# Kernel tuning notes

Hardware: AMD Instinct MI355X
Metric: run time of the kernel (lower is better)

The kernel has to match this reference:

```python
import jax, jax.numpy as jnp
import numpy as np

# geometry constants (mirrors geo dict in init_kwargs)
N_DETEC_U = 512
VIEWS = 360
N_VOX_X = 128
N_VOX_Y = 128
EXTENT = 1
CHANNEL = 8
RANGE_X = 5            # self.range_x_num
R = 2 * RANGE_X + 1    # 11 interpolation taps per sample


def conv1d(x, w, b):
    # x: [N, Cin, L], w: [Cout, Cin, K], padding=1 (same)
    y = jax.lax.conv_general_dilated(
        x, w, window_strides=(1,), padding=((1, 1),),
        dimension_numbers=("NCH", "OIH", "NCH"))
    return y + b[None, :, None]


def setup_inputs() -> dict:
    key = jax.random.key(0)
    k1, k2, k3, k4, k5, k6 = jax.random.split(key, 6)
    B = 2
    hidden = R * CHANNEL * 2   # 176
    out_ch = R * CHANNEL       # 88
    inp = jax.random.normal(k1, (B, CHANNEL, VIEWS, N_DETEC_U), dtype=jnp.float32)
    # indices live in [0, views*nDetecU - 2) so low_ind+1 / high_ind+1 stay in range
    max_idx = float(VIEWS * N_DETEC_U - 2)
    indices = jax.random.uniform(k2, (N_VOX_X * N_VOX_Y * VIEWS * EXTENT,),
                                 dtype=jnp.float32) * max_idx
    fc1_w = jax.random.normal(k3, (hidden, CHANNEL, 3), dtype=jnp.float32) * 0.05
    fc1_b = jax.random.normal(k4, (hidden,), dtype=jnp.float32) * 0.05
    fc2_w = jax.random.normal(k5, (out_ch, hidden, 3), dtype=jnp.float32) * 0.05
    fc2_b = jax.random.normal(k6, (out_ch,), dtype=jnp.float32) * 0.05
    return {"input": inp, "indices": indices, "fc1_w": fc1_w, "fc1_b": fc1_b,
            "fc2_w": fc2_w, "fc2_b": fc2_b}


def reference(input, indices, fc1_w, fc1_b, fc2_w, fc2_b):
    B, C, V, D = input.shape  # [B, channel, views, nDetecU]
    # ---- Mlp (Conv1d -> GELU -> Conv1d) applied per (batch, view) slice ----
    x = jnp.transpose(input, (0, 2, 1, 3)).reshape(B * V, C, D)  # [B*V, C, D]
    h = jax.nn.gelu(conv1d(x, fc1_w, fc1_b), approximate=False)
    y = conv1d(h, fc2_w, fc2_b)                                   # [B*V, R*C, D]
    y = jnp.transpose(y.reshape(B, V, R * C, D), (0, 2, 1, 3))    # [B, R*C, V, D]
    # split R taps to last axis: [B, C, V, D, R] -> flatten last three
    out = jnp.transpose(y.reshape(B, C, R, V, D), (0, 1, 3, 4, 2)).reshape(B, C, V * D * R)
    L = V * D * R
    # ---- back-projection interpolation index math ----
    idx_low = jnp.floor(indices)
    w = indices - idx_low                       # torch.frac (indices >= 0)
    fw = jnp.floor(w * RANGE_X)
    low_ind = idx_low * R + RANGE_X + fw
    low_w = w * RANGE_X - fw                    # frac(weight * range_x_num)
    high_ind = low_ind + RANGE_X + 1
    high_ind = jnp.where(high_ind >= L - 1, float(L - 2), high_ind)
    li = low_ind.astype(jnp.int32)
    hi = high_ind.astype(jnp.int32)
    low = out[:, :, li] * (1.0 - low_w) + out[:, :, li + 1] * low_w
    high = out[:, :, hi] * (1.0 - low_w) + out[:, :, hi + 1] * low_w
    res = low * (1.0 - w) + high * w            # [B, C, Nvox*views*extent]
    return res.reshape(B, C, N_VOX_X * N_VOX_Y, V * EXTENT)
```

## Files before the change

### kernel.cpp

```cpp
#include <hip/hip_runtime.h>
#include <hip/hip_fp16.h>
#include <math.h>

#define VIEWS  360
#define NDET   512
#define CH     8
#define RR     11
#define HID    176
#define OC     88
#define LPOS   (VIEWS*NDET*RR)
#define NIDX   (128*128*VIEWS)

#define DCHUNK 128
#define NCHUNK (NDET/DCHUNK)
#define HTROWS (DCHUNK+2)
#define HTHALF 192
#define NMT    6
#define NKSTEP 18

typedef _Float16 f16x8 __attribute__((ext_vector_type(8)));
typedef float    f32x4 __attribute__((ext_vector_type(4)));

__device__ __align__(16) _Float16 g_w2a[NKSTEP*NMT*64*8];

__device__ __forceinline__ int swz(int r) { return (r ^ (r >> 3)) & 7; }

__global__ __launch_bounds__(256) void pack_w2(const float* __restrict__ w2)
{
    int idx = blockIdx.x*256 + threadIdx.x;
    if (idx >= NKSTEP*NMT*64*8) return;
    int j     = idx & 7;
    int lane  = (idx >> 3) & 63;
    int t     = idx >> 9;
    int mt    = t % NMT;
    int kstep = t / NMT;
    int kb    = kstep / 3, tap = kstep % 3;
    int o     = mt*16 + (lane & 15);
    int hh    = kb*32 + (lane >> 4)*8 + j;
    float v   = (o < OC && hh < HID) ? w2[(o*HID + hh)*3 + tap] : 0.f;
    g_w2a[idx] = (_Float16)v;
}

__global__ __launch_bounds__(256, 2) void mlp_kernel(
    const float* __restrict__ input,
    const float* __restrict__ w1,
    const float* __restrict__ b1,
    const float* __restrict__ b2,
    __half* __restrict__ ws)
{
    const int v    = blockIdx.x;
    const int b    = blockIdx.y;
    const int tid  = threadIdx.x;
    const int lane = tid & 63;
    const int wv   = tid >> 6;
    const int l15  = lane & 15;
    const int l4   = lane >> 4;

    __shared__ __align__(16) float    x_s[520][8];
    __shared__ __align__(16) _Float16 w1_s[HID][24];
    __shared__ float                  b1_s[HID];
    __shared__ __align__(16) _Float16 hT[HTROWS * HTHALF];

    {
        int4 zi = make_int4(0,0,0,0);
        for (int i = tid; i < (HTROWS*HTHALF*2)/16; i += 256) ((int4*)hT)[i] = zi;
    }
    for (int j = tid; j < CH*NDET; j += 256) {
        int c = j >> 9, d = j & 511;
        x_s[d + 2][c] = input[((b*CH + c)*VIEWS + v)*NDET + d];
    }
    if (tid < 64) {
        int t = tid >> 3;
        int row = (t < 2) ? t : 512 + t;
        x_s[row][tid & 7] = 0.f;
    }
    for (int i = tid; i < HID*24; i += 256) w1_s[i/24][i%24] = (_Float16)w1[i];
    for (int i = tid; i < HID;    i += 256) b1_s[i] = b1[i];

    float accb[NMT][4];
    #pragma unroll
    for (int mt = 0; mt < NMT; ++mt)
        #pragma unroll
        for (int q = 0; q < 4; ++q) {
            int o = mt*16 + l4*4 + q;
            accb[mt][q] = (o < OC) ? b2[o] : 0.f;
        }

    __syncthreads();

    for (int chunk = 0; chunk < NCHUNK; ++chunk) {
        const int d0 = chunk * DCHUNK;

        #pragma unroll 1
        for (int it = 0; it < 3; ++it) {
            int i = it*256 + tid;
            if (i < 726) {
                int oct = i / 33;
                int rg  = i - oct*33;
                int r0  = rg * 4;
                float xr[6][8];
                #pragma unroll
                for (int k = 0; k < 6; ++k) {
                    const float4* xp = (const float4*)(&x_s[d0 + r0 + k][0]);
                    float4 xa = xp[0], xb = xp[1];
                    xr[k][0]=xa.x; xr[k][1]=xa.y; xr[k][2]=xa.z; xr[k][3]=xa.w;
                    xr[k][4]=xb.x; xr[k][5]=xb.y; xr[k][6]=xb.z; xr[k][7]=xb.w;
                }
                f16x8 hout[4];
                #pragma unroll
                for (int hsub = 0; hsub < 8; ++hsub) {
                    int hh = oct*8 + hsub;
                    const f16x8* wp = (const f16x8*)(&w1_s[hh][0]);
                    f16x8 wA = wp[0], wB = wp[1], wC = wp[2];
                    float wr[24];
                    #pragma unroll
                    for (int t = 0; t < 8; ++t) {
                        wr[t] = (float)wA[t]; wr[8+t] = (float)wB[t]; wr[16+t] = (float)wC[t];
                    }
                    float bias = b1_s[hh];
                    #pragma unroll
                    for (int rr = 0; rr < 4; ++rr) {
                        float a = bias;
                        #pragma unroll
                        for (int c = 0; c < CH; ++c) {
                            a += wr[c*3+0] * xr[rr+0][c]
                               + wr[c*3+1] * xr[rr+1][c]
                               + wr[c*3+2] * xr[rr+2][c];
                        }
                        int d = d0 - 1 + r0 + rr;
                        float g = 0.f;
                        if ((unsigned)d < (unsigned)NDET)
                            g = 0.5f * a * (1.0f + erff(a * 0.70710678118654752f));
                        hout[rr][hsub] = (_Float16)g;
                    }
                }
                #pragma unroll
                for (int rr = 0; rr < 4; ++rr) {
                    int r = r0 + rr;
                    if (r < HTROWS) {
                        int g = oct ^ swz(r);
                        *(f16x8*)(&hT[r*HTHALF + g*8]) = hout[rr];
                    }
                }
            }
        }
        __syncthreads();

        f32x4 acc[NMT][2];
        #pragma unroll
        for (int mt = 0; mt < NMT; ++mt)
            #pragma unroll
            for (int nt = 0; nt < 2; ++nt)
                #pragma unroll
                for (int q = 0; q < 4; ++q)
                    acc[mt][nt][q] = accb[mt][q];

        #pragma unroll 2
        for (int kb = 0; kb < 6; ++kb) {
            #pragma unroll
            for (int tap = 0; tap < 3; ++tap) {
                const int kstep = kb*3 + tap;
                f16x8 af[NMT];
                #pragma unroll
                for (int mt = 0; mt < NMT; ++mt)
                    af[mt] = *(const f16x8*)(&g_w2a[((kstep*NMT + mt)*64 + lane)*8]);
                f16x8 bf[2];
                #pragma unroll
                for (int nt = 0; nt < 2; ++nt) {
                    int rr = wv*32 + nt*16 + l15 + tap;
                    int g  = (kb*4 + l4) ^ swz(rr);
                    bf[nt] = *(const f16x8*)(&hT[rr*HTHALF + g*8]);
                }
                #pragma unroll
                for (int mt = 0; mt < NMT; ++mt)
                    #pragma unroll
                    for (int nt = 0; nt < 2; ++nt)
                        acc[mt][nt] = __builtin_amdgcn_mfma_f32_16x16x32_f16(
                            af[mt], bf[nt], acc[mt][nt], 0, 0, 0);
            }
        }

        #pragma unroll
        for (int mt = 0; mt < NMT; ++mt) {
            #pragma unroll
            for (int q = 0; q < 4; ++q) {
                int o = mt*16 + l4*4 + q;
                if (o < OC) {
                    int c = o / RR;
                    int r = o - c*RR;
                    #pragma unroll
                    for (int nt = 0; nt < 2; ++nt) {
                        int d = d0 + wv*32 + nt*16 + l15;
                        size_t pos = (size_t)((v*NDET + d)*RR + r);
                        ws[pos*16 + b*8 + c] = __float2half(acc[mt][nt][q]);
                    }
                }
            }
        }
        __syncthreads();
    }
}

__global__ __launch_bounds__(256) void gather_kernel(
    const float* __restrict__ indices,
    const __half* __restrict__ ws,
    float* __restrict__ out)
{
    int i = blockIdx.x * 256 + threadIdx.x;
    if (i >= NIDX) return;

    float idx      = indices[i];
    float idx_low  = floorf(idx);
    float w        = idx - idx_low;
    float fw       = floorf(w * 5.0f);
    float low_ind  = idx_low * 11.0f + 5.0f + fw;
    float low_w    = w * 5.0f - fw;
    float high_ind = low_ind + 6.0f;
    if (high_ind >= (float)(LPOS - 1)) high_ind = (float)(LPOS - 2);
    int li = (int)low_ind;
    int hi = (int)high_ind;

    const uint4* wsv = (const uint4*)ws;
    float omlw = 1.0f - low_w;
    float omw  = 1.0f - w;

    #pragma unroll
    for (int part = 0; part < 2; ++part) {
        uint4 A  = wsv[(size_t)li * 2 + part];
        uint4 Bv = wsv[(size_t)(li + 1) * 2 + part];
        uint4 Cv = wsv[(size_t)hi * 2 + part];
        uint4 Dv = wsv[(size_t)(hi + 1) * 2 + part];
        const __half* ah = (const __half*)&A;
        const __half* bh = (const __half*)&Bv;
        const __half* ch = (const __half*)&Cv;
        const __half* dh = (const __half*)&Dv;
        #pragma unroll
        for (int j = 0; j < 8; ++j) {
            float a  = __half2float(ah[j]);
            float bb = __half2float(bh[j]);
            float cc = __half2float(ch[j]);
            float dd = __half2float(dh[j]);
            float lo = a  * omlw + bb * low_w;
            float hv = cc * omlw + dd * low_w;
            float r  = lo * omw + hv * w;
            out[(size_t)(part * 8 + j) * NIDX + i] = r;
        }
    }
}

extern "C" void kernel_launch(void* const* d_in, const int* in_sizes, int n_in,
                              void* d_out, int out_size, void* d_ws, size_t ws_size,
                              hipStream_t stream) {
    const float* input   = (const float*)d_in[0];
    const float* indices = (const float*)d_in[1];
    const float* w1      = (const float*)d_in[2];
    const float* b1      = (const float*)d_in[3];
    const float* w2      = (const float*)d_in[4];
    const float* b2      = (const float*)d_in[5];
    __half* ws = (__half*)d_ws;
    float* out = (float*)d_out;

    pack_w2<<<dim3((NKSTEP*NMT*64*8 + 255)/256), dim3(256), 0, stream>>>(w2);
    mlp_kernel<<<dim3(VIEWS, 2), dim3(256), 0, stream>>>(input, w1, b1, b2, ws);

    int nb = (NIDX + 255) / 256;
    gather_kernel<<<dim3(nb), dim3(256), 0, stream>>>(indices, ws, out);
}
```

Measured before the change: 930.1 us.

## Halve MLP chunk, stage epilogue in LDS for vector stores, use nontemporal gather IO

Cuts the d-chunk from 128 to 64 so shared memory shrinks and the launch bound allows three blocks per CU. The epilogue no longer writes scattered single halves to the workspace. It first transposes the accumulators through LDS, reusing the hT buffer, and then writes 8-channel f16x8 vectors per position. The gather kernel switches to nontemporal loads of indices and nontemporal stores of outputs to reduce cache pollution. Smaller chunks add more barriers and relatively more halo recomputation.

```diff
diff --git a/kernel.cpp b/kernel.cpp
--- a/kernel.cpp
+++ b/kernel.cpp
@@ -11,12 +11,13 @@
 #define LPOS   (VIEWS*NDET*RR)
 #define NIDX   (128*128*VIEWS)
 
-#define DCHUNK 128
+#define DCHUNK 64
 #define NCHUNK (NDET/DCHUNK)
 #define HTROWS (DCHUNK+2)
 #define HTHALF 192
 #define NMT    6
 #define NKSTEP 18
+#define EPITCH 98
 
 typedef _Float16 f16x8 __attribute__((ext_vector_type(8)));
 typedef float    f32x4 __attribute__((ext_vector_type(4)));
@@ -41,7 +42,7 @@
     g_w2a[idx] = (_Float16)v;
 }
 
-__global__ __launch_bounds__(256, 2) void mlp_kernel(
+__global__ __launch_bounds__(256, 3) void mlp_kernel(
     const float* __restrict__ input,
     const float* __restrict__ w1,
     const float* __restrict__ b1,
@@ -60,6 +61,7 @@
     __shared__ __align__(16) _Float16 w1_s[HID][24];
     __shared__ float                  b1_s[HID];
     __shared__ __align__(16) _Float16 hT[HTROWS * HTHALF];
+    _Float16* eT = hT;
 
     {
         int4 zi = make_int4(0,0,0,0);
@@ -92,11 +94,11 @@
         const int d0 = chunk * DCHUNK;
 
         #pragma unroll 1
-        for (int it = 0; it < 3; ++it) {
+        for (int it = 0; it < 2; ++it) {
             int i = it*256 + tid;
-            if (i < 726) {
-                int oct = i / 33;
-                int rg  = i - oct*33;
+            if (i < 374) {
+                int oct = i / 17;
+                int rg  = i - oct*17;
                 int r0  = rg * 4;
                 float xr[6][8];
                 #pragma unroll
@@ -146,16 +148,14 @@
         }
         __syncthreads();
 
-        f32x4 acc[NMT][2];
+        f32x4 acc[NMT];
         #pragma unroll
         for (int mt = 0; mt < NMT; ++mt)
             #pragma unroll
-            for (int nt = 0; nt < 2; ++nt)
-                #pragma unroll
-                for (int q = 0; q < 4; ++q)
-                    acc[mt][nt][q] = accb[mt][q];
-
-        #pragma unroll 2
+            for (int q = 0; q < 4; ++q)
+                acc[mt][q] = accb[mt][q];
+
+        #pragma unroll 3
         for (int kb = 0; kb < 6; ++kb) {
             #pragma unroll
             for (int tap = 0; tap < 3; ++tap) {
@@ -164,37 +164,42 @@
                 #pragma unroll
                 for (int mt = 0; mt < NMT; ++mt)
                     af[mt] = *(const f16x8*)(&g_w2a[((kstep*NMT + mt)*64 + lane)*8]);
-                f16x8 bf[2];
-                #pragma unroll
-                for (int nt = 0; nt < 2; ++nt) {
-                    int rr = wv*32 + nt*16 + l15 + tap;
-                    int g  = (kb*4 + l4) ^ swz(rr);
-                    bf[nt] = *(const f16x8*)(&hT[rr*HTHALF + g*8]);
-                }
+                int rr = wv*16 + l15 + tap;
+                int g  = (kb*4 + l4) ^ swz(rr);
+                f16x8 bf = *(const f16x8*)(&hT[rr*HTHALF + g*8]);
                 #pragma unroll
                 for (int mt = 0; mt < NMT; ++mt)
-                    #pragma unroll
-                    for (int nt = 0; nt < 2; ++nt)
-                        acc[mt][nt] = __builtin_amdgcn_mfma_f32_16x16x32_f16(
-                            af[mt], bf[nt], acc[mt][nt], 0, 0, 0);
-            }
-        }
-
-        #pragma unroll
-        for (int mt = 0; mt < NMT; ++mt) {
+                    acc[mt] = __builtin_amdgcn_mfma_f32_16x16x32_f16(
+                        af[mt], bf, acc[mt], 0, 0, 0);
+            }
+        }
+        __syncthreads();
+
+        {
+            int d16 = wv*16 + l15;
             #pragma unroll
-            for (int q = 0; q < 4; ++q) {
-                int o = mt*16 + l4*4 + q;
-                if (o < OC) {
-                    int c = o / RR;
-                    int r = o - c*RR;
-                    #pragma unroll
-                    for (int nt = 0; nt < 2; ++nt) {
-                        int d = d0 + wv*32 + nt*16 + l15;
-                        size_t pos = (size_t)((v*NDET + d)*RR + r);
-                        ws[pos*16 + b*8 + c] = __float2half(acc[mt][nt][q]);
-                    }
-                }
+            for (int mt = 0; mt < NMT; ++mt) {
+                #pragma unroll
+                for (int q = 0; q < 4; ++q) {
+                    int o = mt*16 + l4*4 + q;
+                    eT[d16*EPITCH + o] = (_Float16)acc[mt][q];
+                }
+            }
+        }
+        __syncthreads();
+
+        #pragma unroll 1
+        for (int it = 0; it < 3; ++it) {
+            int j = it*256 + tid;
+            if (j < 704) {
+                int d = (j * 2979) >> 15;
+                int r = j - d*11;
+                f16x8 val;
+                #pragma unroll
+                for (int c = 0; c < CH; ++c)
+                    val[c] = eT[d*EPITCH + c*11 + r];
+                size_t pos = (size_t)((v*NDET + d0 + d)*RR + r);
+                *(f16x8*)((__half*)ws + pos*16 + b*8) = val;
             }
         }
         __syncthreads();
@@ -209,7 +214,7 @@
     int i = blockIdx.x * 256 + threadIdx.x;
     if (i >= NIDX) return;
 
-    float idx      = indices[i];
+    float idx      = __builtin_nontemporal_load(&indices[i]);
     float idx_low  = floorf(idx);
     float w        = idx - idx_low;
     float fw       = floorf(w * 5.0f);
@@ -243,7 +248,7 @@
             float lo = a  * omlw + bb * low_w;
             float hv = cc * omlw + dd * low_w;
             float r  = lo * omw + hv * w;
-            out[(size_t)(part * 8 + j) * NIDX + i] = r;
+            __builtin_nontemporal_store(r, &out[(size_t)(part * 8 + j) * NIDX + i]);
         }
     }
 }
```

New measurement: 827.1 us. 11.1% less time.
